# Kernel optimization log

Measured on AMD Instinct MI355X. Metric: run time of the kernel, lower is better.

## Reference

```python
import jax, jax.numpy as jnp
import numpy as np

N_NODES = 100000
N_EDGES = 1600000
D_IN = 128
D_HID = 128


def setup_inputs() -> dict:
    key = jax.random.key(0)
    ks = jax.random.split(key, 8)
    scale_in = 1.0 / np.sqrt(D_IN)
    scale_h = 1.0 / np.sqrt(D_HID)
    return {
        "x": jax.random.normal(ks[0], (N_NODES, D_IN), dtype=jnp.float32),
        "edge_index": jax.random.randint(ks[1], (2, N_EDGES), 0, N_NODES, dtype=jnp.int64),
        "W_l1": jax.random.normal(ks[2], (D_IN, D_HID), dtype=jnp.float32) * scale_in,
        "W_r1": jax.random.normal(ks[3], (D_IN, D_HID), dtype=jnp.float32) * scale_in,
        "b1": jnp.zeros((D_HID,), dtype=jnp.float32),
        "W_l2": jax.random.normal(ks[4], (D_HID, D_HID), dtype=jnp.float32) * scale_h,
        "W_r2": jax.random.normal(ks[5], (D_HID, D_HID), dtype=jnp.float32) * scale_h,
        "b2": jnp.zeros((D_HID,), dtype=jnp.float32),
    }


def _sage_conv(h, src, dst, n_nodes, W_l, W_r, b):
    # mean aggregation of source-node features onto destination nodes
    msg = h[src]                                         # [E, d] gather
    agg = jax.ops.segment_sum(msg, dst, num_segments=n_nodes)   # [N, d]
    cnt = jax.ops.segment_sum(jnp.ones((src.shape[0], 1), h.dtype), dst,
                              num_segments=n_nodes)      # [N, 1]
    mean = agg / jnp.maximum(cnt, 1.0)                   # zero where no in-edges
    return mean @ W_l + b + h @ W_r                      # lin_l(mean) + lin_r(x)


def reference(x, edge_index, W_l1, W_r1, b1, W_l2, W_r2, b2):
    src, dst = edge_index[0], edge_index[1]
    n = x.shape[0]
    h = jax.nn.relu(_sage_conv(x, src, dst, n, W_l1, W_r1, b1))
    # dropout is identity in eval mode
    return _sage_conv(h, src, dst, n, W_l2, W_r2, b2)
```

## Files before the change

kernel.cpp:

```cpp
#include <hip/hip_runtime.h>
#include <stdint.h>

#define N_NODES 100000
#define N_EDGES 1600000
#define D 128
#define NBUCK 196
#define BSTRIDE 9216
#define PCHUNK 2048
#define NTILES (N_NODES / 16)
#define GRID_GEMM 2048
#define CAST_BLOCKS (N_NODES * D / 8 / 256)

typedef unsigned int uint32;
typedef __attribute__((ext_vector_type(8))) short short8;
typedef __attribute__((ext_vector_type(4))) float f32x4;

__device__ __forceinline__ unsigned short f2bf(float f) {
  unsigned u = __builtin_bit_cast(unsigned, f);
  u += 0x7fffu + ((u >> 16) & 1u);
  return (unsigned short)(u >> 16);
}
__device__ __forceinline__ float bflo(unsigned v) {
  return __builtin_bit_cast(float, v << 16);
}
__device__ __forceinline__ float bfhi(unsigned v) {
  return __builtin_bit_cast(float, v & 0xffff0000u);
}


__global__ __launch_bounds__(256) void k_part(const int* __restrict__ src,
                                              const int* __restrict__ dst,
                                              int* __restrict__ bcnt,
                                              uint2* __restrict__ pairs) {
  __shared__ uint2 buff[PCHUNK];
  __shared__ uint2 sorted[PCHUNK];
  __shared__ int hist[256], stmp[256], loff[256], cpos[256], base[256];
  int tid = threadIdx.x;
  int e0 = blockIdx.x * PCHUNK;
  int nv = N_EDGES - e0;
  if (nv > PCHUNK) nv = PCHUNK;

  hist[tid] = 0;
  __syncthreads();
  for (int i = tid; i < nv; i += 256) {
    int d = dst[e0 + i];
    int s = src[e0 + i];
    buff[i] = make_uint2((uint32)d, (uint32)s);
    atomicAdd(&hist[d >> 9], 1);
  }
  __syncthreads();
  int v = hist[tid];
  stmp[tid] = v;
  __syncthreads();
  for (int off = 1; off < 256; off <<= 1) {
    int t = (tid >= off) ? stmp[tid - off] : 0;
    __syncthreads();
    stmp[tid] += t;
    __syncthreads();
  }
  loff[tid] = stmp[tid] - v;
  cpos[tid] = stmp[tid] - v;
  base[tid] = (v > 0) ? atomicAdd(&bcnt[tid], v) : 0;
  __syncthreads();
  for (int i = tid; i < nv; i += 256) {
    uint2 p = buff[i];
    int r = atomicAdd(&cpos[p.x >> 9], 1);
    sorted[r] = p;
  }
  __syncthreads();
  for (int i = tid; i < nv; i += 256) {
    uint2 p = sorted[i];
    int b = (int)(p.x >> 9);
    int local = base[b] + (i - loff[b]);
    if (local < BSTRIDE)
      pairs[(size_t)b * BSTRIDE + local] = p;
  }
}

__global__ __launch_bounds__(512) void k_csr(const uint2* __restrict__ pairs,
                                             const int* __restrict__ bcnt,
                                             int* __restrict__ rowptr,
                                             int* __restrict__ csr) {
  __shared__ int hist[512], off[512], cur[512], scn[512];
  int b = blockIdx.x;
  int tid = threadIdx.x;

  int bv = (tid < NBUCK) ? bcnt[tid] : 0;
  scn[tid] = bv;
  __syncthreads();
  for (int o = 1; o < 512; o <<= 1) {
    int t = (tid >= o) ? scn[tid - o] : 0;
    __syncthreads();
    scn[tid] += t;
    __syncthreads();
  }
  int bb = (b == 0) ? 0 : scn[b - 1];
  if (b == NBUCK - 1 && tid == 0) rowptr[N_NODES] = scn[NBUCK - 1];

  int lo = b << 9;
  int hi = lo + 512;
  if (hi > N_NODES) hi = N_NODES;
  int ne = bcnt[b];
  if (ne > BSTRIDE) ne = BSTRIDE;
  const uint2* pb = pairs + (size_t)b * BSTRIDE;

  hist[tid] = 0;
  __syncthreads();
  for (int i = tid; i < ne; i += 512) atomicAdd(&hist[(int)pb[i].x - lo], 1);
  __syncthreads();
  int v = hist[tid];
  off[tid] = v;
  __syncthreads();
  for (int o = 1; o < 512; o <<= 1) {
    int t = (tid >= o) ? off[tid - o] : 0;
    __syncthreads();
    off[tid] += t;
    __syncthreads();
  }
  off[tid] -= v;
  cur[tid] = off[tid];
  if (lo + tid < hi) rowptr[lo + tid] = bb + off[tid];
  __syncthreads();
  for (int i = tid; i < ne; i += 512) {
    int d = (int)pb[i].x - lo;
    int slot = atomicAdd(&cur[d], 1);
    csr[bb + slot] = (int)pb[i].y;
  }
}


__global__ __launch_bounds__(256) void k_prep(
    const float* __restrict__ x, unsigned short* __restrict__ xb,
    const float* __restrict__ Wl1, const float* __restrict__ Wr1,
    const float* __restrict__ Wl2, const float* __restrict__ Wr2,
    unsigned short* __restrict__ Wp1, unsigned short* __restrict__ Wp2) {
  int blk = blockIdx.x;
  int tid = threadIdx.x;
  if (blk < CAST_BLOCKS) {
    int i = blk * 256 + tid;
    float4 a = *reinterpret_cast<const float4*>(x + (size_t)i * 8);
    float4 c = *reinterpret_cast<const float4*>(x + (size_t)i * 8 + 4);
    uint4 o;
    o.x = (uint32)f2bf(a.x) | ((uint32)f2bf(a.y) << 16);
    o.y = (uint32)f2bf(a.z) | ((uint32)f2bf(a.w) << 16);
    o.z = (uint32)f2bf(c.x) | ((uint32)f2bf(c.y) << 16);
    o.w = (uint32)f2bf(c.z) | ((uint32)f2bf(c.w) << 16);
    *reinterpret_cast<uint4*>(xb + (size_t)i * 8) = o;
  } else {
    int t = (blk - CAST_BLOCKS) * 256 + tid;
    int which = t >> 15;
    int tt = t & 32767;
    int j = tt & 7;
    int lane = (tt >> 3) & 63;
    int tile = (tt >> 9) & 1;
    int ks = (tt >> 10) & 7;
    int ng = (tt >> 13) & 3;
    int k = ks * 32 + (lane >> 4) * 8 + j;
    int n = ng * 32 + tile * 16 + (lane & 15);
    const float* Wl = which ? Wl2 : Wl1;
    const float* Wr = which ? Wr2 : Wr1;
    float w = (k < 128) ? Wl[k * 128 + n] : Wr[(k - 128) * 128 + n];
    (which ? Wp2 : Wp1)[tt] = f2bf(w);
  }
}


#define ACC8(v)                                          \
  acc[0] += bflo(v.x); acc[1] += bfhi(v.x);              \
  acc[2] += bflo(v.y); acc[3] += bfhi(v.y);              \
  acc[4] += bflo(v.z); acc[5] += bfhi(v.z);              \
  acc[6] += bflo(v.w); acc[7] += bfhi(v.w);

__global__ __launch_bounds__(256, 6) void k_mean(
    const unsigned short* __restrict__ table,
    const int* __restrict__ rowptr, const int* __restrict__ csr,
    unsigned short* __restrict__ meanb) {
  int g = threadIdx.x >> 4;
  int l = threadIdx.x & 15;
  int node = blockIdx.x * 16 + g;
  int beg = rowptr[node], end = rowptr[node + 1];
  float acc[8] = {0.f, 0.f, 0.f, 0.f, 0.f, 0.f, 0.f, 0.f};
  int e = beg;
  for (; e + 8 <= end; e += 8) {
    int s0 = csr[e], s1 = csr[e + 1], s2 = csr[e + 2], s3 = csr[e + 3];
    int s4 = csr[e + 4], s5 = csr[e + 5], s6 = csr[e + 6], s7 = csr[e + 7];
    uint4 v0 = *reinterpret_cast<const uint4*>(table + (size_t)s0 * D + l * 8);
    uint4 v1 = *reinterpret_cast<const uint4*>(table + (size_t)s1 * D + l * 8);
    uint4 v2 = *reinterpret_cast<const uint4*>(table + (size_t)s2 * D + l * 8);
    uint4 v3 = *reinterpret_cast<const uint4*>(table + (size_t)s3 * D + l * 8);
    uint4 v4 = *reinterpret_cast<const uint4*>(table + (size_t)s4 * D + l * 8);
    uint4 v5 = *reinterpret_cast<const uint4*>(table + (size_t)s5 * D + l * 8);
    uint4 v6 = *reinterpret_cast<const uint4*>(table + (size_t)s6 * D + l * 8);
    uint4 v7 = *reinterpret_cast<const uint4*>(table + (size_t)s7 * D + l * 8);
    ACC8(v0) ACC8(v1) ACC8(v2) ACC8(v3)
    ACC8(v4) ACC8(v5) ACC8(v6) ACC8(v7)
  }
  for (; e + 4 <= end; e += 4) {
    int s0 = csr[e], s1 = csr[e + 1], s2 = csr[e + 2], s3 = csr[e + 3];
    uint4 v0 = *reinterpret_cast<const uint4*>(table + (size_t)s0 * D + l * 8);
    uint4 v1 = *reinterpret_cast<const uint4*>(table + (size_t)s1 * D + l * 8);
    uint4 v2 = *reinterpret_cast<const uint4*>(table + (size_t)s2 * D + l * 8);
    uint4 v3 = *reinterpret_cast<const uint4*>(table + (size_t)s3 * D + l * 8);
    ACC8(v0) ACC8(v1) ACC8(v2) ACC8(v3)
  }
  for (; e < end; ++e) {
    int s0 = csr[e];
    uint4 v0 = *reinterpret_cast<const uint4*>(table + (size_t)s0 * D + l * 8);
    ACC8(v0)
  }
  float inv = (end > beg) ? 1.0f / (float)(end - beg) : 0.0f;
  uint4 o;
  o.x = (uint32)f2bf(acc[0] * inv) | ((uint32)f2bf(acc[1] * inv) << 16);
  o.y = (uint32)f2bf(acc[2] * inv) | ((uint32)f2bf(acc[3] * inv) << 16);
  o.z = (uint32)f2bf(acc[4] * inv) | ((uint32)f2bf(acc[5] * inv) << 16);
  o.w = (uint32)f2bf(acc[6] * inv) | ((uint32)f2bf(acc[7] * inv) << 16);
  *reinterpret_cast<uint4*>(meanb + (size_t)node * D + l * 8) = o;
}

__global__ __launch_bounds__(256) void k_gemm(
    const unsigned short* __restrict__ xrows,
    const unsigned short* __restrict__ mrows,
    const unsigned short* __restrict__ Wp, const float* __restrict__ bias,
    void* __restrict__ outp, int relu_bf16_out) {
  int tid = threadIdx.x;
  int wave = tid >> 6;
  int lane = tid & 63;
  int q = lane >> 4;
  int r = lane & 15;

  short8 Bf[8][2];
  const unsigned short* wp = Wp + ((size_t)wave * 8 * 2) * 64 * 8 + lane * 8;
#pragma unroll
  for (int ks = 0; ks < 8; ++ks)
#pragma unroll
    for (int t = 0; t < 2; ++t)
      Bf[ks][t] = *reinterpret_cast<const short8*>(wp + (ks * 2 + t) * 512);

  float bia0 = bias[wave * 32 + r];
  float bia1 = bias[wave * 32 + 16 + r];

  for (int tile = blockIdx.x; tile < NTILES; tile += GRID_GEMM) {
    int n0 = tile * 16;
    const unsigned short* am = mrows + (size_t)(n0 + r) * D + q * 8;
    const unsigned short* ax = xrows + (size_t)(n0 + r) * D + q * 8;
    short8 A[8];
#pragma unroll
    for (int ks = 0; ks < 4; ++ks)
      A[ks] = *reinterpret_cast<const short8*>(am + ks * 32);
#pragma unroll
    for (int ks = 0; ks < 4; ++ks)
      A[4 + ks] = *reinterpret_cast<const short8*>(ax + ks * 32);

    f32x4 c0 = {0.f, 0.f, 0.f, 0.f}, c1 = {0.f, 0.f, 0.f, 0.f};
#pragma unroll
    for (int ks = 0; ks < 8; ++ks) {
      c0 = __builtin_amdgcn_mfma_f32_16x16x32_bf16(A[ks], Bf[ks][0], c0, 0, 0, 0);
      c1 = __builtin_amdgcn_mfma_f32_16x16x32_bf16(A[ks], Bf[ks][1], c1, 0, 0, 0);
    }

    int orow = n0 + q * 4;
    if (relu_bf16_out) {
      unsigned short* ob = (unsigned short*)outp + (size_t)orow * D + wave * 32 + r;
#pragma unroll
      for (int gg = 0; gg < 4; ++gg) {
        ob[(size_t)gg * D] = f2bf(fmaxf(c0[gg] + bia0, 0.f));
        ob[(size_t)gg * D + 16] = f2bf(fmaxf(c1[gg] + bia1, 0.f));
      }
    } else {
      float* of = (float*)outp + (size_t)orow * D + wave * 32 + r;
#pragma unroll
      for (int gg = 0; gg < 4; ++gg) {
        of[(size_t)gg * D] = c0[gg] + bia0;
        of[(size_t)gg * D + 16] = c1[gg] + bia1;
      }
    }
  }
}


extern "C" void kernel_launch(void* const* d_in, const int* in_sizes, int n_in,
                              void* d_out, int out_size, void* d_ws, size_t ws_size,
                              hipStream_t stream) {
  const float* x   = (const float*)d_in[0];
  const int*   ei  = (const int*)d_in[1];
  const float* Wl1 = (const float*)d_in[2];
  const float* Wr1 = (const float*)d_in[3];
  const float* b1  = (const float*)d_in[4];
  const float* Wl2 = (const float*)d_in[5];
  const float* Wr2 = (const float*)d_in[6];
  const float* b2  = (const float*)d_in[7];
  float* out = (float*)d_out;

  const int* esrc = ei;
  const int* edst = ei + N_EDGES;

  char* p = (char*)d_ws;
  auto take = [&](size_t bytes) {
    char* q = p;
    p += (bytes + 255) & ~(size_t)255;
    return q;
  };
  int* bcnt   = (int*)take(256 * 4);
  int* rowptr = (int*)take((size_t)(N_NODES + 1) * 4);
  int* csr    = (int*)take((size_t)N_EDGES * 4);
  size_t pairs_bytes = (size_t)NBUCK * BSTRIDE * 8;
  size_t meanb_bytes = (size_t)N_NODES * D * 2;
  char* unionbuf = (char*)take(pairs_bytes > meanb_bytes ? pairs_bytes : meanb_bytes);
  uint2* pairs = (uint2*)unionbuf;
  unsigned short* meanb = (unsigned short*)unionbuf;
  unsigned short* xb  = (unsigned short*)take((size_t)N_NODES * D * 2);
  unsigned short* hb  = (unsigned short*)take((size_t)N_NODES * D * 2);
  unsigned short* Wp1 = (unsigned short*)take(256 * 128 * 2);
  unsigned short* Wp2 = (unsigned short*)take(256 * 128 * 2);

  const int npart = (N_EDGES + PCHUNK - 1) / PCHUNK;

  hipMemsetAsync(bcnt, 0, 256 * 4, stream);
  k_part<<<npart, 256, 0, stream>>>(esrc, edst, bcnt, pairs);
  k_csr<<<NBUCK, 512, 0, stream>>>(pairs, bcnt, rowptr, csr);

  k_prep<<<CAST_BLOCKS + 256, 256, 0, stream>>>(x, xb, Wl1, Wr1, Wl2, Wr2, Wp1, Wp2);

  k_mean<<<NTILES, 256, 0, stream>>>(xb, rowptr, csr, meanb);
  k_gemm<<<GRID_GEMM, 256, 0, stream>>>(xb, meanb, Wp1, b1, hb, 1);
  k_mean<<<NTILES, 256, 0, stream>>>(hb, rowptr, csr, meanb);
  k_gemm<<<GRID_GEMM, 256, 0, stream>>>(hb, meanb, Wp2, b2, out, 0);
}
```

Measured before the change: 326.6 us.

## Fuse mean aggregation with GEMM via LDS and merge CSR build with casting

Mean aggregation and the SAGE linear layer now run in one kernel per layer. Each 512-thread block computes 32 node means into an XOR-swizzled LDS tile and then feeds them straight into MFMA, so the bf16 mean buffer no longer makes a round trip through global memory. The CSR build and the x/weight bf16 cast-and-pack are merged into one launch with disjoint block roles, which cuts the launch count. The cost is that every block reloads the packed weight fragments and the fused kernel has higher register and LDS pressure, which may reduce occupancy.

```diff
diff --git a/kernel.cpp b/kernel.cpp
--- a/kernel.cpp
+++ b/kernel.cpp
@@ -7,9 +7,9 @@
 #define NBUCK 196
 #define BSTRIDE 9216
 #define PCHUNK 2048
-#define NTILES (N_NODES / 16)
-#define GRID_GEMM 2048
-#define CAST_BLOCKS (N_NODES * D / 8 / 256)
+#define NTILE32 (N_NODES / 32)
+#define CASTB 3125
+#define WPACKB 128
 
 typedef unsigned int uint32;
 typedef __attribute__((ext_vector_type(8))) short short8;
@@ -77,14 +77,49 @@
   }
 }
 
-__global__ __launch_bounds__(512) void k_csr(const uint2* __restrict__ pairs,
-                                             const int* __restrict__ bcnt,
-                                             int* __restrict__ rowptr,
-                                             int* __restrict__ csr) {
+__global__ __launch_bounds__(512) void k_csr_prep(
+    const uint2* __restrict__ pairs, const int* __restrict__ bcnt,
+    int* __restrict__ rowptr, int* __restrict__ csr,
+    const float* __restrict__ x, unsigned short* __restrict__ xb,
+    const float* __restrict__ Wl1, const float* __restrict__ Wr1,
+    const float* __restrict__ Wl2, const float* __restrict__ Wr2,
+    unsigned short* __restrict__ Wp1, unsigned short* __restrict__ Wp2) {
   __shared__ int hist[512], off[512], cur[512], scn[512];
-  int b = blockIdx.x;
   int tid = threadIdx.x;
-
+  int blk = blockIdx.x;
+
+  if (blk >= NBUCK) {
+    int pb = blk - NBUCK;
+    if (pb < CASTB) {
+      size_t i = (size_t)pb * 512 + tid;
+      float4 a = *reinterpret_cast<const float4*>(x + i * 8);
+      float4 c = *reinterpret_cast<const float4*>(x + i * 8 + 4);
+      uint4 o;
+      o.x = (uint32)f2bf(a.x) | ((uint32)f2bf(a.y) << 16);
+      o.y = (uint32)f2bf(a.z) | ((uint32)f2bf(a.w) << 16);
+      o.z = (uint32)f2bf(c.x) | ((uint32)f2bf(c.y) << 16);
+      o.w = (uint32)f2bf(c.z) | ((uint32)f2bf(c.w) << 16);
+      *reinterpret_cast<uint4*>(xb + i * 8) = o;
+    } else {
+      int t = (pb - CASTB) * 512 + tid;
+      int which = t >> 15;
+      int tt = t & 32767;
+      int j = tt & 7;
+      int lane = (tt >> 3) & 63;
+      int tile = (tt >> 9) & 1;
+      int ks = (tt >> 10) & 7;
+      int ng = (tt >> 13) & 3;
+      int k = ks * 32 + (lane >> 4) * 8 + j;
+      int n = ng * 32 + tile * 16 + (lane & 15);
+      const float* Wl = which ? Wl2 : Wl1;
+      const float* Wr = which ? Wr2 : Wr1;
+      float w = (k < 128) ? Wl[k * 128 + n] : Wr[(k - 128) * 128 + n];
+      (which ? Wp2 : Wp1)[tt] = f2bf(w);
+    }
+    return;
+  }
+
+  int b = blk;
   int bv = (tid < NBUCK) ? bcnt[tid] : 0;
   scn[tid] = bv;
   __syncthreads();
@@ -102,11 +137,11 @@
   if (hi > N_NODES) hi = N_NODES;
   int ne = bcnt[b];
   if (ne > BSTRIDE) ne = BSTRIDE;
-  const uint2* pb = pairs + (size_t)b * BSTRIDE;
+  const uint2* pb2 = pairs + (size_t)b * BSTRIDE;
 
   hist[tid] = 0;
   __syncthreads();
-  for (int i = tid; i < ne; i += 512) atomicAdd(&hist[(int)pb[i].x - lo], 1);
+  for (int i = tid; i < ne; i += 512) atomicAdd(&hist[(int)pb2[i].x - lo], 1);
   __syncthreads();
   int v = hist[tid];
   off[tid] = v;
@@ -122,45 +157,9 @@
   if (lo + tid < hi) rowptr[lo + tid] = bb + off[tid];
   __syncthreads();
   for (int i = tid; i < ne; i += 512) {
-    int d = (int)pb[i].x - lo;
+    int d = (int)pb2[i].x - lo;
     int slot = atomicAdd(&cur[d], 1);
-    csr[bb + slot] = (int)pb[i].y;
-  }
-}
-
-
-__global__ __launch_bounds__(256) void k_prep(
-    const float* __restrict__ x, unsigned short* __restrict__ xb,
-    const float* __restrict__ Wl1, const float* __restrict__ Wr1,
-    const float* __restrict__ Wl2, const float* __restrict__ Wr2,
-    unsigned short* __restrict__ Wp1, unsigned short* __restrict__ Wp2) {
-  int blk = blockIdx.x;
-  int tid = threadIdx.x;
-  if (blk < CAST_BLOCKS) {
-    int i = blk * 256 + tid;
-    float4 a = *reinterpret_cast<const float4*>(x + (size_t)i * 8);
-    float4 c = *reinterpret_cast<const float4*>(x + (size_t)i * 8 + 4);
-    uint4 o;
-    o.x = (uint32)f2bf(a.x) | ((uint32)f2bf(a.y) << 16);
-    o.y = (uint32)f2bf(a.z) | ((uint32)f2bf(a.w) << 16);
-    o.z = (uint32)f2bf(c.x) | ((uint32)f2bf(c.y) << 16);
-    o.w = (uint32)f2bf(c.z) | ((uint32)f2bf(c.w) << 16);
-    *reinterpret_cast<uint4*>(xb + (size_t)i * 8) = o;
-  } else {
-    int t = (blk - CAST_BLOCKS) * 256 + tid;
-    int which = t >> 15;
-    int tt = t & 32767;
-    int j = tt & 7;
-    int lane = (tt >> 3) & 63;
-    int tile = (tt >> 9) & 1;
-    int ks = (tt >> 10) & 7;
-    int ng = (tt >> 13) & 3;
-    int k = ks * 32 + (lane >> 4) * 8 + j;
-    int n = ng * 32 + tile * 16 + (lane & 15);
-    const float* Wl = which ? Wl2 : Wl1;
-    const float* Wr = which ? Wr2 : Wr1;
-    float w = (k < 128) ? Wl[k * 128 + n] : Wr[(k - 128) * 128 + n];
-    (which ? Wp2 : Wp1)[tt] = f2bf(w);
+    csr[bb + slot] = (int)pb2[i].y;
   }
 }
 
@@ -171,13 +170,18 @@
   acc[4] += bflo(v.z); acc[5] += bfhi(v.z);              \
   acc[6] += bflo(v.w); acc[7] += bfhi(v.w);
 
-__global__ __launch_bounds__(256, 6) void k_mean(
+__global__ __launch_bounds__(512, 4) void k_fused(
     const unsigned short* __restrict__ table,
     const int* __restrict__ rowptr, const int* __restrict__ csr,
-    unsigned short* __restrict__ meanb) {
-  int g = threadIdx.x >> 4;
-  int l = threadIdx.x & 15;
-  int node = blockIdx.x * 16 + g;
+    const unsigned short* __restrict__ Wp, const float* __restrict__ bias,
+    void* __restrict__ outp, int relu_bf16_out) {
+  __shared__ unsigned short meanB[32 * 128];
+  int tid = threadIdx.x;
+  int g = tid >> 4;
+  int l = tid & 15;
+  int tile = blockIdx.x;
+  int node = tile * 32 + g;
+
   int beg = rowptr[node], end = rowptr[node + 1];
   float acc[8] = {0.f, 0.f, 0.f, 0.f, 0.f, 0.f, 0.f, 0.f};
   int e = beg;
@@ -214,65 +218,59 @@
   o.y = (uint32)f2bf(acc[2] * inv) | ((uint32)f2bf(acc[3] * inv) << 16);
   o.z = (uint32)f2bf(acc[4] * inv) | ((uint32)f2bf(acc[5] * inv) << 16);
   o.w = (uint32)f2bf(acc[6] * inv) | ((uint32)f2bf(acc[7] * inv) << 16);
-  *reinterpret_cast<uint4*>(meanb + (size_t)node * D + l * 8) = o;
-}
-
-__global__ __launch_bounds__(256) void k_gemm(
-    const unsigned short* __restrict__ xrows,
-    const unsigned short* __restrict__ mrows,
-    const unsigned short* __restrict__ Wp, const float* __restrict__ bias,
-    void* __restrict__ outp, int relu_bf16_out) {
-  int tid = threadIdx.x;
+  *reinterpret_cast<uint4*>(&meanB[g * 128 + (l ^ (g & 15)) * 8]) = o;
+  __syncthreads();
+
   int wave = tid >> 6;
   int lane = tid & 63;
+  int wr = wave >> 2;
+  int wc = wave & 3;
   int q = lane >> 4;
   int r = lane & 15;
 
   short8 Bf[8][2];
-  const unsigned short* wp = Wp + ((size_t)wave * 8 * 2) * 64 * 8 + lane * 8;
+  const unsigned short* wp = Wp + (size_t)wc * 8192 + lane * 8;
 #pragma unroll
   for (int ks = 0; ks < 8; ++ks)
 #pragma unroll
     for (int t = 0; t < 2; ++t)
       Bf[ks][t] = *reinterpret_cast<const short8*>(wp + (ks * 2 + t) * 512);
 
-  float bia0 = bias[wave * 32 + r];
-  float bia1 = bias[wave * 32 + 16 + r];
-
-  for (int tile = blockIdx.x; tile < NTILES; tile += GRID_GEMM) {
-    int n0 = tile * 16;
-    const unsigned short* am = mrows + (size_t)(n0 + r) * D + q * 8;
-    const unsigned short* ax = xrows + (size_t)(n0 + r) * D + q * 8;
-    short8 A[8];
-#pragma unroll
-    for (int ks = 0; ks < 4; ++ks)
-      A[ks] = *reinterpret_cast<const short8*>(am + ks * 32);
-#pragma unroll
-    for (int ks = 0; ks < 4; ++ks)
-      A[4 + ks] = *reinterpret_cast<const short8*>(ax + ks * 32);
-
-    f32x4 c0 = {0.f, 0.f, 0.f, 0.f}, c1 = {0.f, 0.f, 0.f, 0.f};
-#pragma unroll
-    for (int ks = 0; ks < 8; ++ks) {
-      c0 = __builtin_amdgcn_mfma_f32_16x16x32_bf16(A[ks], Bf[ks][0], c0, 0, 0, 0);
-      c1 = __builtin_amdgcn_mfma_f32_16x16x32_bf16(A[ks], Bf[ks][1], c1, 0, 0, 0);
+  int arow = wr * 16 + r;
+  short8 A[8];
+  const unsigned short* ax = table + (size_t)(tile * 32 + arow) * D + q * 8;
+#pragma unroll
+  for (int ks = 0; ks < 4; ++ks)
+    A[4 + ks] = *reinterpret_cast<const short8*>(ax + ks * 32);
+#pragma unroll
+  for (int ks = 0; ks < 4; ++ks) {
+    int slot = (ks * 4 + q) ^ r;
+    A[ks] = *reinterpret_cast<const short8*>(&meanB[arow * 128 + slot * 8]);
+  }
+
+  f32x4 c0 = {0.f, 0.f, 0.f, 0.f}, c1 = {0.f, 0.f, 0.f, 0.f};
+#pragma unroll
+  for (int ks = 0; ks < 8; ++ks) {
+    c0 = __builtin_amdgcn_mfma_f32_16x16x32_bf16(A[ks], Bf[ks][0], c0, 0, 0, 0);
+    c1 = __builtin_amdgcn_mfma_f32_16x16x32_bf16(A[ks], Bf[ks][1], c1, 0, 0, 0);
+  }
+
+  float bia0 = bias[wc * 32 + r];
+  float bia1 = bias[wc * 32 + 16 + r];
+  int orow = tile * 32 + wr * 16 + q * 4;
+  if (relu_bf16_out) {
+    unsigned short* ob = (unsigned short*)outp + (size_t)orow * D + wc * 32 + r;
+#pragma unroll
+    for (int gg = 0; gg < 4; ++gg) {
+      ob[(size_t)gg * D] = f2bf(fmaxf(c0[gg] + bia0, 0.f));
+      ob[(size_t)gg * D + 16] = f2bf(fmaxf(c1[gg] + bia1, 0.f));
     }
-
-    int orow = n0 + q * 4;
-    if (relu_bf16_out) {
-      unsigned short* ob = (unsigned short*)outp + (size_t)orow * D + wave * 32 + r;
-#pragma unroll
-      for (int gg = 0; gg < 4; ++gg) {
-        ob[(size_t)gg * D] = f2bf(fmaxf(c0[gg] + bia0, 0.f));
-        ob[(size_t)gg * D + 16] = f2bf(fmaxf(c1[gg] + bia1, 0.f));
-      }
-    } else {
-      float* of = (float*)outp + (size_t)orow * D + wave * 32 + r;
-#pragma unroll
-      for (int gg = 0; gg < 4; ++gg) {
-        of[(size_t)gg * D] = c0[gg] + bia0;
-        of[(size_t)gg * D + 16] = c1[gg] + bia1;
-      }
+  } else {
+    float* of = (float*)outp + (size_t)orow * D + wc * 32 + r;
+#pragma unroll
+    for (int gg = 0; gg < 4; ++gg) {
+      of[(size_t)gg * D] = c0[gg] + bia0;
+      of[(size_t)gg * D + 16] = c1[gg] + bia1;
     }
   }
 }
@@ -303,11 +301,7 @@
   int* bcnt   = (int*)take(256 * 4);
   int* rowptr = (int*)take((size_t)(N_NODES + 1) * 4);
   int* csr    = (int*)take((size_t)N_EDGES * 4);
-  size_t pairs_bytes = (size_t)NBUCK * BSTRIDE * 8;
-  size_t meanb_bytes = (size_t)N_NODES * D * 2;
-  char* unionbuf = (char*)take(pairs_bytes > meanb_bytes ? pairs_bytes : meanb_bytes);
-  uint2* pairs = (uint2*)unionbuf;
-  unsigned short* meanb = (unsigned short*)unionbuf;
+  uint2* pairs = (uint2*)take((size_t)NBUCK * BSTRIDE * 8);
   unsigned short* xb  = (unsigned short*)take((size_t)N_NODES * D * 2);
   unsigned short* hb  = (unsigned short*)take((size_t)N_NODES * D * 2);
   unsigned short* Wp1 = (unsigned short*)take(256 * 128 * 2);
@@ -317,12 +311,9 @@
 
   hipMemsetAsync(bcnt, 0, 256 * 4, stream);
   k_part<<<npart, 256, 0, stream>>>(esrc, edst, bcnt, pairs);
-  k_csr<<<NBUCK, 512, 0, stream>>>(pairs, bcnt, rowptr, csr);
-
-  k_prep<<<CAST_BLOCKS + 256, 256, 0, stream>>>(x, xb, Wl1, Wr1, Wl2, Wr2, Wp1, Wp2);
-
-  k_mean<<<NTILES, 256, 0, stream>>>(xb, rowptr, csr, meanb);
-  k_gemm<<<GRID_GEMM, 256, 0, stream>>>(xb, meanb, Wp1, b1, hb, 1);
-  k_mean<<<NTILES, 256, 0, stream>>>(hb, rowptr, csr, meanb);
-  k_gemm<<<GRID_GEMM, 256, 0, stream>>>(hb, meanb, Wp2, b2, out, 0);
-}
+  k_csr_prep<<<NBUCK + CASTB + WPACKB, 512, 0, stream>>>(
+      pairs, bcnt, rowptr, csr, x, xb, Wl1, Wr1, Wl2, Wr2, Wp1, Wp2);
+
+  k_fused<<<NTILE32, 512, 0, stream>>>(xb, rowptr, csr, Wp1, b1, hb, 1);
+  k_fused<<<NTILE32, 512, 0, stream>>>(hb, rowptr, csr, Wp2, b2, out, 0);
+}
```

Result: faster. 319.0 us (-2.3%).
